# Optimization experiments

Hardware: AMD Instinct MI355X
Metric: run time of the kernel (lower is better)

The kernel has to match this reference:

```python
import jax, jax.numpy as jnp
import numpy as np

B, C, D, H, W = 2, 32, 96, 96, 96
RED = 16
INV_SQRT2 = 0.7071067811865476  # 1/sqrt(2), Haar analysis filter coefficient
BN_EPS = 1e-5


def _haar1(x, axis):
    # pywt 'haar' DWT on even-length signals: a[i]=(x[2i]+x[2i+1])/sqrt2, d[i]=(x[2i]-x[2i+1])/sqrt2
    e = jax.lax.slice_in_dim(x, 0, None, stride=2, axis=axis)
    o = jax.lax.slice_in_dim(x, 1, None, stride=2, axis=axis)
    return (e + o) * INV_SQRT2, (e - o) * INV_SQRT2


def haar_dwt3d(x):
    # x: (B, C, D, H, W). Separable 3D Haar DWT; key letters follow pywt dwtn
    # axis order (D, H, W): 'aad' = approx along D, approx along H, detail along W.
    aD, dD = _haar1(x, 2)
    aa, ad = _haar1(aD, 3)
    da, dd = _haar1(dD, 3)
    aaa, aad = _haar1(aa, 4)
    ada, add = _haar1(ad, 4)
    daa, dad = _haar1(da, 4)
    dda, ddd = _haar1(dd, 4)
    # per-channel grouping of 7 detail bands, then flatten to (B, 7C, D/2, H/2, W/2)
    high = jnp.stack([aad, ada, add, daa, dad, dda, ddd], axis=2)
    b, c = x.shape[0], x.shape[1]
    high = high.reshape(b, c * 7, *aaa.shape[2:])
    return aaa, high


def chan_attn(x, w1, w2):
    # AdaptiveAvgPool3d(1) -> FC(no bias) -> ReLU -> FC(no bias) -> Sigmoid -> scale
    y = x.mean(axis=(2, 3, 4))                     # (B, Ch)
    y = jax.nn.sigmoid(jnp.maximum(y @ w1.T, 0.0) @ w2.T)
    return x * y[:, :, None, None, None]


def setup_inputs() -> dict:
    key = jax.random.key(0)
    ks = jax.random.split(key, 7)
    x = jax.random.normal(ks[0], (B, C, D, H, W), dtype=jnp.float32)
    w1_low = jax.random.normal(ks[1], (C // RED, C), dtype=jnp.float32) * 0.1
    w2_low = jax.random.normal(ks[2], (C, C // RED), dtype=jnp.float32) * 0.1
    w1_high = jax.random.normal(ks[3], (7 * C // RED, 7 * C), dtype=jnp.float32) * 0.05
    w2_high = jax.random.normal(ks[4], (7 * C, 7 * C // RED), dtype=jnp.float32) * 0.05
    w_fuse = jax.random.normal(ks[5], (C, 8 * C), dtype=jnp.float32) * 0.05  # 1x1x1 conv kernel
    b_fuse = jnp.zeros((C,), dtype=jnp.float32)
    gamma = jnp.ones((C,), dtype=jnp.float32)
    beta = jnp.zeros((C,), dtype=jnp.float32)
    return dict(x=x, w1_low=w1_low, w2_low=w2_low, w1_high=w1_high, w2_high=w2_high,
                w_fuse=w_fuse, b_fuse=b_fuse, gamma=gamma, beta=beta)


def reference(x, w1_low, w2_low, w1_high, w2_high, w_fuse, b_fuse, gamma, beta):
    low, high = haar_dwt3d(x)                                  # (B,C,48,48,48), (B,7C,48,48,48)
    low = chan_attn(low, w1_low, w2_low)
    high = chan_attn(high, w1_high, w2_high)
    z = jnp.concatenate([low, high], axis=1)                   # (B, 8C, 48,48,48)
    z = jnp.einsum('bcdhw,oc->bodhw', z, w_fuse) + b_fuse[None, :, None, None, None]
    # BatchNorm3d (training-mode batch statistics, as fresh torch module defaults)
    mu = z.mean(axis=(0, 2, 3, 4), keepdims=True)
    var = z.var(axis=(0, 2, 3, 4), keepdims=True)
    z = (z - mu) * jax.lax.rsqrt(var + BN_EPS)
    z = z * gamma[None, :, None, None, None] + beta[None, :, None, None, None]
    return jnp.maximum(z, 0.0)
```

## Files before the change

### kernel.cpp

```cpp
#include <hip/hip_runtime.h>
#include <math.h>

#define HS 0.35355339059327373f
#define NSPAT 110592
#define NBN   221184

__global__ __launch_bounds__(256) void k1_parity(const float* __restrict__ x,
                                                 float* __restrict__ S) {
    int blk = blockIdx.x;
    int d   = blk % 96;
    int bc  = blk / 96;
    const float4* x4 = (const float4*)x + (long)blk * 2304;
    int tid = threadIdx.x;
    float aE0 = 0.f, aO0 = 0.f, aE1 = 0.f, aO1 = 0.f;
#pragma unroll
    for (int i = 0; i < 9; ++i) {
        int f = tid + i * 256;
        float4 v = x4[f];
        int h = f / 24;
        float e = v.x + v.z, o = v.y + v.w;
        if (h & 1) { aE1 += e; aO1 += o; }
        else       { aE0 += e; aO0 += o; }
    }
#pragma unroll
    for (int m = 32; m; m >>= 1) {
        aE0 += __shfl_xor(aE0, m, 64); aO0 += __shfl_xor(aO0, m, 64);
        aE1 += __shfl_xor(aE1, m, 64); aO1 += __shfl_xor(aO1, m, 64);
    }
    __shared__ float red[4][4];
    int lane = tid & 63, wave = tid >> 6;
    if (lane == 0) { red[wave][0] = aE0; red[wave][1] = aO0;
                     red[wave][2] = aE1; red[wave][3] = aO1; }
    __syncthreads();
    if (tid < 4) {
        float v = red[0][tid] + red[1][tid] + red[2][tid] + red[3][tid];
        int q = tid >> 1, r = tid & 1, p = d & 1;
        atomicAdd(&S[bc * 8 + p * 4 + q * 2 + r], v);
    }
}

__global__ __launch_bounds__(256) void k2_attn(
        const float* __restrict__ S,
        const float* __restrict__ w1l, const float* __restrict__ w2l,
        const float* __restrict__ w1h, const float* __restrict__ w2h,
        const float* __restrict__ wf, float* __restrict__ A) {
    int b = blockIdx.x, tid = threadIdx.x;
    __shared__ float mlow[32], mhigh[224], h1l[2], h1h[14], ylow[32], yhigh[224];
    const float* Sb = S + b * 256;
    const float MS = HS / (float)NSPAT;
    if (tid < 32) {
        float s = 0.f;
        for (int j = 0; j < 8; ++j) s += Sb[tid * 8 + j];
        mlow[tid] = s * MS;
    }
    if (tid < 224) {
        int c = tid / 7, k = tid % 7, dm = k + 1;
        float s = 0.f;
        for (int j = 0; j < 8; ++j) {
            float sg = (__popc(j & dm) & 1) ? -1.f : 1.f;
            s += sg * Sb[c * 8 + j];
        }
        mhigh[tid] = s * MS;
    }
    __syncthreads();
    if (tid < 2) {
        float s = 0.f;
        for (int c = 0; c < 32; ++c) s += w1l[tid * 32 + c] * mlow[c];
        h1l[tid] = fmaxf(s, 0.f);
    } else if (tid < 16) {
        int j = tid - 2;
        float s = 0.f;
        for (int c = 0; c < 224; ++c) s += w1h[j * 224 + c] * mhigh[c];
        h1h[j] = fmaxf(s, 0.f);
    }
    __syncthreads();
    if (tid < 32) {
        float s = w2l[tid * 2] * h1l[0] + w2l[tid * 2 + 1] * h1l[1];
        ylow[tid] = 1.f / (1.f + expf(-s));
    } else if (tid < 256) {
        int i = tid - 32;
        float s = 0.f;
        for (int j = 0; j < 14; ++j) s += w2h[i * 14 + j] * h1h[j];
        yhigh[i] = 1.f / (1.f + expf(-s));
    }
    __syncthreads();
    for (int idx = tid; idx < 8192; idx += 256) {
        int o = idx >> 8, c = (idx >> 3) & 31, pqr = idx & 7;
        float a = wf[o * 256 + c] * ylow[c];
#pragma unroll
        for (int k = 0; k < 7; ++k) {
            float sg = (__popc(pqr & (k + 1)) & 1) ? -1.f : 1.f;
            a += sg * wf[o * 256 + 32 + c * 7 + k] * yhigh[c * 7 + k];
        }
        int og = o >> 3, op = o & 7;
        A[b * 8192 + (og * 32 + c) * 64 + op * 8 + pqr] = a * HS;
    }
}

__global__ __launch_bounds__(192) void k3_main(const float* __restrict__ x,
                                               const float* __restrict__ A,
                                               float* __restrict__ z,
                                               float* __restrict__ bnSum,
                                               float* __restrict__ bnSq) {
    __shared__ float red[3][16];
    int blk  = blockIdx.x;
    int og   = blk / 576;
    int rem  = blk % 576;
    int ohg  = rem % 6;
    int tmp  = rem / 6;
    int od   = tmp % 48;
    int b    = tmp / 48;
    int tid  = threadIdx.x;
    int row  = tid / 24;
    int t    = tid % 24;
    int oh   = ohg * 8 + row;

    const float* Ab = A + b * 8192 + og * 2048;

    float acc0[8], acc1[8];
#pragma unroll
    for (int o = 0; o < 8; ++o) { acc0[o] = 0.f; acc1[o] = 0.f; }

    const float4* x4 = (const float4*)x;
    int base = (((b * 32) * 96 + 2 * od) * 96 + 2 * oh) * 24 + t;

    float4 v00 = x4[base];
    float4 v01 = x4[base + 24];
    float4 v10 = x4[base + 2304];
    float4 v11 = x4[base + 2328];
    for (int c = 0; c < 32; ++c) {
        float4 n00, n01, n10, n11;
        if (c < 31) {
            int i4 = base + (c + 1) * 221184;
            n00 = x4[i4];
            n01 = x4[i4 + 24];
            n10 = x4[i4 + 2304];
            n11 = x4[i4 + 2328];
        }
        const float* Ac = Ab + c * 64;
#pragma unroll
        for (int o = 0; o < 8; ++o) {
            const float* Ao = Ac + o * 8;
            float a0 = Ao[0], a1 = Ao[1], a2 = Ao[2], a3 = Ao[3];
            float a4 = Ao[4], a5 = Ao[5], a6 = Ao[6], a7 = Ao[7];
            acc0[o] += a0 * v00.x + a1 * v00.y + a2 * v01.x + a3 * v01.y
                     + a4 * v10.x + a5 * v10.y + a6 * v11.x + a7 * v11.y;
            acc1[o] += a0 * v00.z + a1 * v00.w + a2 * v01.z + a3 * v01.w
                     + a4 * v10.z + a5 * v10.w + a6 * v11.z + a7 * v11.w;
        }
        v00 = n00; v01 = n01; v10 = n10; v11 = n11;
    }

    float2* z2 = (float2*)z;
#pragma unroll
    for (int o = 0; o < 8; ++o) {
        int zi = (((b * 32 + og * 8 + o) * 48 + od) * 48 + oh) * 24 + t;
        z2[zi] = make_float2(acc0[o], acc1[o]);
    }

    int lane = tid & 63, wave = tid >> 6;
#pragma unroll
    for (int o = 0; o < 8; ++o) {
        float sv = acc0[o] + acc1[o];
        float qv = acc0[o] * acc0[o] + acc1[o] * acc1[o];
#pragma unroll
        for (int m = 32; m; m >>= 1) {
            sv += __shfl_xor(sv, m, 64);
            qv += __shfl_xor(qv, m, 64);
        }
        if (lane == 0) { red[wave][o] = sv; red[wave][8 + o] = qv; }
    }
    __syncthreads();
    if (tid < 16) {
        float v = red[0][tid] + red[1][tid] + red[2][tid];
        if (tid < 8) atomicAdd(&bnSum[og * 8 + tid], v);
        else         atomicAdd(&bnSq[og * 8 + tid - 8], v);
    }
}

__global__ __launch_bounds__(256) void k5_norm(float* __restrict__ z,
                                               const float* __restrict__ bnSum,
                                               const float* __restrict__ bnSq,
                                               const float* __restrict__ gamma,
                                               const float* __restrict__ beta) {
    __shared__ float s_sc[32], s_sh[32];
    int tid = threadIdx.x;
    if (tid < 32) {
        const float invN = 1.f / (float)NBN;
        float mean = bnSum[tid] * invN;
        float var  = bnSq[tid] * invN - mean * mean;
        float inv  = rsqrtf(var + 1e-5f);
        float sc   = gamma[tid] * inv;
        s_sc[tid] = sc;
        s_sh[tid] = beta[tid] - mean * sc;
    }
    int i = blockIdx.x * 256 + tid;
    float4* z4 = (float4*)z;
    float4 v = z4[i];
    __syncthreads();
    int o = (i / 27648) & 31;
    float sc = s_sc[o], sh = s_sh[o];
    v.x = fmaxf(v.x * sc + sh, 0.f);
    v.y = fmaxf(v.y * sc + sh, 0.f);
    v.z = fmaxf(v.z * sc + sh, 0.f);
    v.w = fmaxf(v.w * sc + sh, 0.f);
    z4[i] = v;
}

extern "C" void kernel_launch(void* const* d_in, const int* in_sizes, int n_in,
                              void* d_out, int out_size, void* d_ws, size_t ws_size,
                              hipStream_t stream) {
    const float* x    = (const float*)d_in[0];
    const float* w1l  = (const float*)d_in[1];
    const float* w2l  = (const float*)d_in[2];
    const float* w1h  = (const float*)d_in[3];
    const float* w2h  = (const float*)d_in[4];
    const float* wf   = (const float*)d_in[5];
    const float* gamma = (const float*)d_in[7];
    const float* beta  = (const float*)d_in[8];
    float* out = (float*)d_out;

    float* ws    = (float*)d_ws;
    float* S     = ws;
    float* bnSum = ws + 512;
    float* bnSq  = ws + 544;
    float* A     = ws + 1024;

    hipMemsetAsync(d_ws, 0, 576 * sizeof(float), stream);
    k1_parity<<<6144, 256, 0, stream>>>(x, S);
    k2_attn<<<2, 256, 0, stream>>>(S, w1l, w2l, w1h, w2h, wf, A);
    k3_main<<<2304, 192, 0, stream>>>(x, A, out, bnSum, bnSq);
    k5_norm<<<6912, 256, 0, stream>>>(out, bnSum, bnSq, gamma, beta);
}
```

Before: 456.3 us.

## Restructure fused conv to compute all 32 outputs per thread with split-K over waves

The main kernel now assigns each lane one output voxel and all 32 output channels, and splits the 32 input channels across the 4 waves of a block. Partial sums are reduced through shared memory and written as float4. This means each input element is read once instead of once per output-channel group (previously 4 reads). BatchNorm statistics now go into 16 replicated atomic slots to reduce contention, and the normalization kernel sums those slots. In exchange the kernel uses 32 accumulator registers, a large shared-memory buffer, and an extra sync.

```diff
diff --git a/kernel.cpp b/kernel.cpp
--- a/kernel.cpp
+++ b/kernel.cpp
@@ -92,103 +92,104 @@
             float sg = (__popc(pqr & (k + 1)) & 1) ? -1.f : 1.f;
             a += sg * wf[o * 256 + 32 + c * 7 + k] * yhigh[c * 7 + k];
         }
-        int og = o >> 3, op = o & 7;
-        A[b * 8192 + (og * 32 + c) * 64 + op * 8 + pqr] = a * HS;
-    }
-}
-
-__global__ __launch_bounds__(192) void k3_main(const float* __restrict__ x,
+        A[b * 8192 + c * 256 + o * 8 + pqr] = a * HS;
+    }
+}
+
+__global__ __launch_bounds__(256) void k3_main(const float* __restrict__ x,
                                                const float* __restrict__ A,
                                                float* __restrict__ z,
-                                               float* __restrict__ bnSum,
-                                               float* __restrict__ bnSq) {
-    __shared__ float red[3][16];
+                                               float* __restrict__ bnRep) {
+    __shared__ float lds[4 * 64 * 33];
     int blk  = blockIdx.x;
-    int og   = blk / 576;
-    int rem  = blk % 576;
-    int ohg  = rem % 6;
-    int tmp  = rem / 6;
+    int vblk = blk % 36;
+    int tmp  = blk / 36;
     int od   = tmp % 48;
     int b    = tmp / 48;
     int tid  = threadIdx.x;
-    int row  = tid / 24;
-    int t    = tid % 24;
-    int oh   = ohg * 8 + row;
-
-    const float* Ab = A + b * 8192 + og * 2048;
-
-    float acc0[8], acc1[8];
-#pragma unroll
-    for (int o = 0; o < 8; ++o) { acc0[o] = 0.f; acc1[o] = 0.f; }
-
-    const float4* x4 = (const float4*)x;
-    int base = (((b * 32) * 96 + 2 * od) * 96 + 2 * oh) * 24 + t;
-
-    float4 v00 = x4[base];
-    float4 v01 = x4[base + 24];
-    float4 v10 = x4[base + 2304];
-    float4 v11 = x4[base + 2328];
-    for (int c = 0; c < 32; ++c) {
-        float4 n00, n01, n10, n11;
-        if (c < 31) {
-            int i4 = base + (c + 1) * 221184;
-            n00 = x4[i4];
-            n01 = x4[i4 + 24];
-            n10 = x4[i4 + 2304];
-            n11 = x4[i4 + 2328];
-        }
-        const float* Ac = Ab + c * 64;
-#pragma unroll
-        for (int o = 0; o < 8; ++o) {
+    int lane = tid & 63;
+    int wv   = __builtin_amdgcn_readfirstlane(tid >> 6);
+    int vbase = vblk * 64;
+    int v    = vbase + lane;
+    int oh   = v / 48, ow = v % 48;
+
+    const float* Ab = A + b * 8192;
+
+    float acc[32];
+#pragma unroll
+    for (int o = 0; o < 32; ++o) acc[o] = 0.f;
+
+    const float2* x2 = (const float2*)x;
+    int base = (b * 32 + wv * 8) * 442368 + od * 9216 + oh * 96 + ow;
+
+    float2 v00 = x2[base], v01 = x2[base + 48];
+    float2 v10 = x2[base + 4608], v11 = x2[base + 4656];
+#pragma unroll
+    for (int i = 0; i < 8; ++i) {
+        float2 n00, n01, n10, n11;
+        if (i < 7) {
+            int nb = base + (i + 1) * 442368;
+            n00 = x2[nb]; n01 = x2[nb + 48];
+            n10 = x2[nb + 4608]; n11 = x2[nb + 4656];
+        }
+        const float* Ac = Ab + (wv * 8 + i) * 256;
+#pragma unroll
+        for (int o = 0; o < 32; ++o) {
             const float* Ao = Ac + o * 8;
-            float a0 = Ao[0], a1 = Ao[1], a2 = Ao[2], a3 = Ao[3];
-            float a4 = Ao[4], a5 = Ao[5], a6 = Ao[6], a7 = Ao[7];
-            acc0[o] += a0 * v00.x + a1 * v00.y + a2 * v01.x + a3 * v01.y
-                     + a4 * v10.x + a5 * v10.y + a6 * v11.x + a7 * v11.y;
-            acc1[o] += a0 * v00.z + a1 * v00.w + a2 * v01.z + a3 * v01.w
-                     + a4 * v10.z + a5 * v10.w + a6 * v11.z + a7 * v11.w;
-        }
-        v00 = n00; v01 = n01; v10 = n10; v11 = n11;
-    }
-
-    float2* z2 = (float2*)z;
-#pragma unroll
-    for (int o = 0; o < 8; ++o) {
-        int zi = (((b * 32 + og * 8 + o) * 48 + od) * 48 + oh) * 24 + t;
-        z2[zi] = make_float2(acc0[o], acc1[o]);
-    }
-
-    int lane = tid & 63, wave = tid >> 6;
-#pragma unroll
-    for (int o = 0; o < 8; ++o) {
-        float sv = acc0[o] + acc1[o];
-        float qv = acc0[o] * acc0[o] + acc1[o] * acc1[o];
-#pragma unroll
-        for (int m = 32; m; m >>= 1) {
-            sv += __shfl_xor(sv, m, 64);
-            qv += __shfl_xor(qv, m, 64);
-        }
-        if (lane == 0) { red[wave][o] = sv; red[wave][8 + o] = qv; }
-    }
-    __syncthreads();
-    if (tid < 16) {
-        float v = red[0][tid] + red[1][tid] + red[2][tid];
-        if (tid < 8) atomicAdd(&bnSum[og * 8 + tid], v);
-        else         atomicAdd(&bnSq[og * 8 + tid - 8], v);
+            acc[o] += Ao[0] * v00.x + Ao[1] * v00.y + Ao[2] * v01.x + Ao[3] * v01.y
+                    + Ao[4] * v10.x + Ao[5] * v10.y + Ao[6] * v11.x + Ao[7] * v11.y;
+        }
+        if (i < 7) { v00 = n00; v01 = n01; v10 = n10; v11 = n11; }
+    }
+
+    float* mine = &lds[(wv * 64 + lane) * 33];
+#pragma unroll
+    for (int o = 0; o < 32; ++o) mine[o] = acc[o];
+    __syncthreads();
+
+    int o = tid >> 3, g = tid & 7;
+    float val[8];
+#pragma unroll
+    for (int j = 0; j < 8; ++j) {
+        int a0 = (g * 8 + j) * 33 + o;
+        val[j] = lds[a0] + lds[2112 + a0] + lds[4224 + a0] + lds[6336 + a0];
+    }
+    int zf = ((b * 32 + o) * 48 + od) * 2304 + vbase + g * 8;
+    float4* z4 = (float4*)(z + zf);
+    z4[0] = make_float4(val[0], val[1], val[2], val[3]);
+    z4[1] = make_float4(val[4], val[5], val[6], val[7]);
+
+    float sv = 0.f, qv = 0.f;
+#pragma unroll
+    for (int j = 0; j < 8; ++j) { sv += val[j]; qv += val[j] * val[j]; }
+#pragma unroll
+    for (int m = 1; m <= 4; m <<= 1) {
+        sv += __shfl_xor(sv, m, 64);
+        qv += __shfl_xor(qv, m, 64);
+    }
+    if ((tid & 7) == 0) {
+        int rep = (blockIdx.x & 15) * 64;
+        atomicAdd(&bnRep[rep + o], sv);
+        atomicAdd(&bnRep[rep + 32 + o], qv);
     }
 }
 
 __global__ __launch_bounds__(256) void k5_norm(float* __restrict__ z,
-                                               const float* __restrict__ bnSum,
-                                               const float* __restrict__ bnSq,
+                                               const float* __restrict__ bnRep,
                                                const float* __restrict__ gamma,
                                                const float* __restrict__ beta) {
     __shared__ float s_sc[32], s_sh[32];
     int tid = threadIdx.x;
     if (tid < 32) {
+        float s = 0.f, q = 0.f;
+#pragma unroll
+        for (int r = 0; r < 16; ++r) {
+            s += bnRep[r * 64 + tid];
+            q += bnRep[r * 64 + 32 + tid];
+        }
         const float invN = 1.f / (float)NBN;
-        float mean = bnSum[tid] * invN;
-        float var  = bnSq[tid] * invN - mean * mean;
+        float mean = s * invN;
+        float var  = q * invN - mean * mean;
         float inv  = rsqrtf(var + 1e-5f);
         float sc   = gamma[tid] * inv;
         s_sc[tid] = sc;
@@ -222,13 +223,12 @@
 
     float* ws    = (float*)d_ws;
     float* S     = ws;
-    float* bnSum = ws + 512;
-    float* bnSq  = ws + 544;
-    float* A     = ws + 1024;
-
-    hipMemsetAsync(d_ws, 0, 576 * sizeof(float), stream);
+    float* bnRep = ws + 512;
+    float* A     = ws + 2048;
+
+    hipMemsetAsync(d_ws, 0, 1536 * sizeof(float), stream);
     k1_parity<<<6144, 256, 0, stream>>>(x, S);
     k2_attn<<<2, 256, 0, stream>>>(S, w1l, w2l, w1h, w2h, wf, A);
-    k3_main<<<2304, 192, 0, stream>>>(x, A, out, bnSum, bnSq);
-    k5_norm<<<6912, 256, 0, stream>>>(out, bnSum, bnSq, gamma, beta);
-}
+    k3_main<<<3456, 256, 0, stream>>>(x, A, out, bnRep);
+    k5_norm<<<6912, 256, 0, stream>>>(out, bnRep, gamma, beta);
+}
```

Result: slower. 493.0 us (+8.0%).

## Widen k3 per-thread tile to four outputs, reorder blocks, replicate BN atomics

Applied to the files above, without the earlier changes.

Each k3 thread now computes four adjacent W outputs (two float4 loads per row) instead of two. This halves the block count, amortises the A-coefficient reads over more FMAs, and stores z as float4. The block index now puts the output-channel group innermost, so the four og blocks sharing the same x slab run close together and reuse it in cache. BatchNorm sum and sum-of-squares atomics are spread across 16 replicas to cut contention, and k5 reduces the replicas. The cost is higher register pressure and fewer blocks for latency hiding.

```diff
diff --git a/kernel.cpp b/kernel.cpp
--- a/kernel.cpp
+++ b/kernel.cpp
@@ -93,49 +93,49 @@
             a += sg * wf[o * 256 + 32 + c * 7 + k] * yhigh[c * 7 + k];
         }
         int og = o >> 3, op = o & 7;
-        A[b * 8192 + (og * 32 + c) * 64 + op * 8 + pqr] = a * HS;
+        A[b * 8192 + og * 2048 + c * 64 + op * 8 + pqr] = a * HS;
     }
 }
 
 __global__ __launch_bounds__(192) void k3_main(const float* __restrict__ x,
                                                const float* __restrict__ A,
                                                float* __restrict__ z,
-                                               float* __restrict__ bnSum,
-                                               float* __restrict__ bnSq) {
+                                               float* __restrict__ bnRep) {
     __shared__ float red[3][16];
-    int blk  = blockIdx.x;
-    int og   = blk / 576;
-    int rem  = blk % 576;
-    int ohg  = rem % 6;
-    int tmp  = rem / 6;
-    int od   = tmp % 48;
-    int b    = tmp / 48;
-    int tid  = threadIdx.x;
-    int row  = tid / 24;
-    int t    = tid % 24;
-    int oh   = ohg * 8 + row;
+    int blk = blockIdx.x;
+    int og  = blk & 3;
+    int rem = blk >> 2;
+    int ohg = rem % 3;
+    int tmp = rem / 3;
+    int od  = tmp % 48;
+    int b   = tmp / 48;
+    int tid = threadIdx.x;
+    int row = tid / 12;
+    int t   = tid % 12;
+    int oh  = ohg * 16 + row;
 
     const float* Ab = A + b * 8192 + og * 2048;
 
-    float acc0[8], acc1[8];
-#pragma unroll
-    for (int o = 0; o < 8; ++o) { acc0[o] = 0.f; acc1[o] = 0.f; }
+    float acc0[8], acc1[8], acc2[8], acc3[8];
+#pragma unroll
+    for (int o = 0; o < 8; ++o) { acc0[o] = 0.f; acc1[o] = 0.f;
+                                  acc2[o] = 0.f; acc3[o] = 0.f; }
 
     const float4* x4 = (const float4*)x;
-    int base = (((b * 32) * 96 + 2 * od) * 96 + 2 * oh) * 24 + t;
-
-    float4 v00 = x4[base];
-    float4 v01 = x4[base + 24];
-    float4 v10 = x4[base + 2304];
-    float4 v11 = x4[base + 2328];
+    int base = (b * 32) * 221184 + (2 * od) * 2304 + (2 * oh) * 24 + 2 * t;
+
+    float4 u00a = x4[base],        u00b = x4[base + 1];
+    float4 u01a = x4[base + 24],   u01b = x4[base + 25];
+    float4 u10a = x4[base + 2304], u10b = x4[base + 2305];
+    float4 u11a = x4[base + 2328], u11b = x4[base + 2329];
     for (int c = 0; c < 32; ++c) {
-        float4 n00, n01, n10, n11;
+        float4 n00a, n00b, n01a, n01b, n10a, n10b, n11a, n11b;
         if (c < 31) {
             int i4 = base + (c + 1) * 221184;
-            n00 = x4[i4];
-            n01 = x4[i4 + 24];
-            n10 = x4[i4 + 2304];
-            n11 = x4[i4 + 2328];
+            n00a = x4[i4];        n00b = x4[i4 + 1];
+            n01a = x4[i4 + 24];   n01b = x4[i4 + 25];
+            n10a = x4[i4 + 2304]; n10b = x4[i4 + 2305];
+            n11a = x4[i4 + 2328]; n11b = x4[i4 + 2329];
         }
         const float* Ac = Ab + c * 64;
 #pragma unroll
@@ -143,26 +143,32 @@
             const float* Ao = Ac + o * 8;
             float a0 = Ao[0], a1 = Ao[1], a2 = Ao[2], a3 = Ao[3];
             float a4 = Ao[4], a5 = Ao[5], a6 = Ao[6], a7 = Ao[7];
-            acc0[o] += a0 * v00.x + a1 * v00.y + a2 * v01.x + a3 * v01.y
-                     + a4 * v10.x + a5 * v10.y + a6 * v11.x + a7 * v11.y;
-            acc1[o] += a0 * v00.z + a1 * v00.w + a2 * v01.z + a3 * v01.w
-                     + a4 * v10.z + a5 * v10.w + a6 * v11.z + a7 * v11.w;
-        }
-        v00 = n00; v01 = n01; v10 = n10; v11 = n11;
-    }
-
-    float2* z2 = (float2*)z;
+            acc0[o] += a0 * u00a.x + a1 * u00a.y + a2 * u01a.x + a3 * u01a.y
+                     + a4 * u10a.x + a5 * u10a.y + a6 * u11a.x + a7 * u11a.y;
+            acc1[o] += a0 * u00a.z + a1 * u00a.w + a2 * u01a.z + a3 * u01a.w
+                     + a4 * u10a.z + a5 * u10a.w + a6 * u11a.z + a7 * u11a.w;
+            acc2[o] += a0 * u00b.x + a1 * u00b.y + a2 * u01b.x + a3 * u01b.y
+                     + a4 * u10b.x + a5 * u10b.y + a6 * u11b.x + a7 * u11b.y;
+            acc3[o] += a0 * u00b.z + a1 * u00b.w + a2 * u01b.z + a3 * u01b.w
+                     + a4 * u10b.z + a5 * u10b.w + a6 * u11b.z + a7 * u11b.w;
+        }
+        u00a = n00a; u00b = n00b; u01a = n01a; u01b = n01b;
+        u10a = n10a; u10b = n10b; u11a = n11a; u11b = n11b;
+    }
+
+    float4* z4 = (float4*)z;
 #pragma unroll
     for (int o = 0; o < 8; ++o) {
-        int zi = (((b * 32 + og * 8 + o) * 48 + od) * 48 + oh) * 24 + t;
-        z2[zi] = make_float2(acc0[o], acc1[o]);
+        int zf = (((b * 32 + og * 8 + o) * 48 + od) * 48 + oh) * 12 + t;
+        z4[zf] = make_float4(acc0[o], acc1[o], acc2[o], acc3[o]);
     }
 
     int lane = tid & 63, wave = tid >> 6;
 #pragma unroll
     for (int o = 0; o < 8; ++o) {
-        float sv = acc0[o] + acc1[o];
-        float qv = acc0[o] * acc0[o] + acc1[o] * acc1[o];
+        float sv = acc0[o] + acc1[o] + acc2[o] + acc3[o];
+        float qv = acc0[o] * acc0[o] + acc1[o] * acc1[o]
+                 + acc2[o] * acc2[o] + acc3[o] * acc3[o];
 #pragma unroll
         for (int m = 32; m; m >>= 1) {
             sv += __shfl_xor(sv, m, 64);
@@ -173,22 +179,28 @@
     __syncthreads();
     if (tid < 16) {
         float v = red[0][tid] + red[1][tid] + red[2][tid];
-        if (tid < 8) atomicAdd(&bnSum[og * 8 + tid], v);
-        else         atomicAdd(&bnSq[og * 8 + tid - 8], v);
+        int rep = (blockIdx.x & 15) * 64;
+        if (tid < 8) atomicAdd(&bnRep[rep + og * 8 + tid], v);
+        else         atomicAdd(&bnRep[rep + 32 + og * 8 + tid - 8], v);
     }
 }
 
 __global__ __launch_bounds__(256) void k5_norm(float* __restrict__ z,
-                                               const float* __restrict__ bnSum,
-                                               const float* __restrict__ bnSq,
+                                               const float* __restrict__ bnRep,
                                                const float* __restrict__ gamma,
                                                const float* __restrict__ beta) {
     __shared__ float s_sc[32], s_sh[32];
     int tid = threadIdx.x;
     if (tid < 32) {
+        float s = 0.f, q = 0.f;
+#pragma unroll
+        for (int r = 0; r < 16; ++r) {
+            s += bnRep[r * 64 + tid];
+            q += bnRep[r * 64 + 32 + tid];
+        }
         const float invN = 1.f / (float)NBN;
-        float mean = bnSum[tid] * invN;
-        float var  = bnSq[tid] * invN - mean * mean;
+        float mean = s * invN;
+        float var  = q * invN - mean * mean;
         float inv  = rsqrtf(var + 1e-5f);
         float sc   = gamma[tid] * inv;
         s_sc[tid] = sc;
@@ -222,13 +234,12 @@
 
     float* ws    = (float*)d_ws;
     float* S     = ws;
-    float* bnSum = ws + 512;
-    float* bnSq  = ws + 544;
-    float* A     = ws + 1024;
-
-    hipMemsetAsync(d_ws, 0, 576 * sizeof(float), stream);
+    float* bnRep = ws + 512;
+    float* A     = ws + 2048;
+
+    hipMemsetAsync(d_ws, 0, 1536 * sizeof(float), stream);
     k1_parity<<<6144, 256, 0, stream>>>(x, S);
     k2_attn<<<2, 256, 0, stream>>>(S, w1l, w2l, w1h, w2h, wf, A);
-    k3_main<<<2304, 192, 0, stream>>>(x, A, out, bnSum, bnSq);
-    k5_norm<<<6912, 256, 0, stream>>>(out, bnSum, bnSq, gamma, beta);
-}
+    k3_main<<<1152, 192, 0, stream>>>(x, A, out, bnRep);
+    k5_norm<<<6912, 256, 0, stream>>>(out, bnRep, gamma, beta);
+}
```

Result: slower. 480.9 us (+5.4%).
